# Kernel optimization log

Measured on AMD Instinct MI355X. Metric: run time of the kernel, lower is better.

Reference implementation:

```python
import jax, jax.numpy as jnp
import numpy as np

N, D = 8192, 4096
DIM_K = 4096

def setup_inputs() -> dict:
    key0 = jax.random.key(0)
    k1, k2, k3 = jax.random.split(key0, 3)
    return {
        "query": jax.random.normal(k1, (N, D), dtype=jnp.float32),
        "key": jax.random.normal(k2, (D, N), dtype=jnp.float32),
        "value": jax.random.normal(k3, (N, D), dtype=jnp.float32),
    }

def reference(query, key, value):
    # Faithful to the (buggy) torch module: ELEMENTWISE query * key.T,
    # scale by sqrt(dim_k), elementwise * value, softmax over dim=1
    # (F.softmax's implicit dim for a 2D tensor). The mask branch in the
    # original (`if x:`) cannot execute for multi-element tensors, so it
    # is omitted (mask=None path).
    scale = jnp.sqrt(jnp.float32(DIM_K))
    x = (query * key.T) / scale  # [N, D]
    x = x * value                # [N, D]
    return jax.nn.softmax(x, axis=1)
```

## Files before the change

### kernel.cpp

```cpp
#include <hip/hip_runtime.h>
#include <math.h>


static constexpr int NROW = 8192;
static constexpr int D    = 4096;
static constexpr int RPB  = 16;
static constexpr int TJ   = 256;
static constexpr int NT   = D / TJ;
static constexpr int LSTR = TJ + 4;

__global__ __launch_bounds__(1024, 2)
void sdp_softmax_kernel(const float* __restrict__ Q,
                        const float* __restrict__ K,
                        const float* __restrict__ V,
                        float* __restrict__ O)
{
    __shared__ float ldsK[2][RPB * LSTR];

    const int tid  = threadIdx.x;
    const int wv   = tid >> 6;
    const int lane = tid & 63;

    const int row0 = blockIdx.x * RPB;
    const int r    = row0 + wv;

    const float* qrow = Q + (size_t)r * D;
    const float* vrow = V + (size_t)r * D;
    float*       orow = O + (size_t)r * D;

    const int il = tid & 15;
    const int jg = tid >> 4;
    const float* kbase = K + (size_t)(4 * jg) * NROW + (size_t)row0 + il;

    float ka = kbase[0];
    float kb = kbase[NROW];
    float kc = kbase[2 * (size_t)NROW];
    float kd = kbase[3 * (size_t)NROW];
    *(float4*)&ldsK[0][il * LSTR + 4 * jg] = make_float4(ka, kb, kc, kd);
    {
        const float* p = kbase + (size_t)TJ * NROW;
        ka = p[0]; kb = p[NROW]; kc = p[2 * (size_t)NROW]; kd = p[3 * (size_t)NROW];
    }
    float4 qv = *(const float4*)(qrow + 4 * lane);
    float4 vv = *(const float4*)(vrow + 4 * lane);
    __syncthreads();

    float4 e0, e1, e2, e3, e4, e5, e6, e7,
           e8, e9, e10, e11, e12, e13, e14, e15;
    float s = 0.0f;

#define TILE_ITER(n, EV)                                                      \
    {                                                                         \
        const float4 kf = *(const float4*)&ldsK[(n) & 1][wv * LSTR + 4*lane]; \
        const float4 qc = qv, vc = vv;                                        \
        if ((n) + 1 < NT) {                                                   \
            *(float4*)&ldsK[((n) + 1) & 1][il * LSTR + 4 * jg] =              \
                make_float4(ka, kb, kc, kd);                                  \
            qv = *(const float4*)(qrow + ((n) + 1) * TJ + 4 * lane);          \
            vv = *(const float4*)(vrow + ((n) + 1) * TJ + 4 * lane);          \
        }                                                                     \
        if ((n) + 2 < NT) {                                                   \
            const float* p = kbase + (size_t)((n) + 2) * TJ * NROW;           \
            ka = p[0]; kb = p[NROW];                                          \
            kc = p[2 * (size_t)NROW]; kd = p[3 * (size_t)NROW];               \
        }                                                                     \
        EV.x = __expf(((qc.x * kf.x) * 0.015625f) * vc.x);                    \
        EV.y = __expf(((qc.y * kf.y) * 0.015625f) * vc.y);                    \
        EV.z = __expf(((qc.z * kf.z) * 0.015625f) * vc.z);                    \
        EV.w = __expf(((qc.w * kf.w) * 0.015625f) * vc.w);                    \
        s += (EV.x + EV.y) + (EV.z + EV.w);                                   \
        if ((n) + 1 < NT) __syncthreads();                                    \
        __builtin_amdgcn_sched_barrier(0);                                    \
    }

    TILE_ITER(0,  e0)  TILE_ITER(1,  e1)  TILE_ITER(2,  e2)  TILE_ITER(3,  e3)
    TILE_ITER(4,  e4)  TILE_ITER(5,  e5)  TILE_ITER(6,  e6)  TILE_ITER(7,  e7)
    TILE_ITER(8,  e8)  TILE_ITER(9,  e9)  TILE_ITER(10, e10) TILE_ITER(11, e11)
    TILE_ITER(12, e12) TILE_ITER(13, e13) TILE_ITER(14, e14) TILE_ITER(15, e15)
#undef TILE_ITER

    #pragma unroll
    for (int i = 1; i < 64; i <<= 1)
        s += __shfl_xor(s, i, 64);
    const float inv = 1.0f / s;

#define WRITE_TILE(n, EV)                                                     \
    {                                                                         \
        float4 xx = EV;                                                       \
        xx.x *= inv; xx.y *= inv; xx.z *= inv; xx.w *= inv;                   \
        *(float4*)(orow + (size_t)(n) * TJ + 4 * lane) = xx;                  \
    }

    WRITE_TILE(0,  e0)  WRITE_TILE(1,  e1)  WRITE_TILE(2,  e2)  WRITE_TILE(3,  e3)
    WRITE_TILE(4,  e4)  WRITE_TILE(5,  e5)  WRITE_TILE(6,  e6)  WRITE_TILE(7,  e7)
    WRITE_TILE(8,  e8)  WRITE_TILE(9,  e9)  WRITE_TILE(10, e10) WRITE_TILE(11, e11)
    WRITE_TILE(12, e12) WRITE_TILE(13, e13) WRITE_TILE(14, e14) WRITE_TILE(15, e15)
#undef WRITE_TILE
}

extern "C" void kernel_launch(void* const* d_in, const int* in_sizes, int n_in,
                              void* d_out, int out_size, void* d_ws, size_t ws_size,
                              hipStream_t stream) {
    const float* Q = (const float*)d_in[0];
    const float* K = (const float*)d_in[1];
    const float* V = (const float*)d_in[2];
    float* O = (float*)d_out;

    dim3 grid(NROW / RPB);
    dim3 block(1024);
    sdp_softmax_kernel<<<grid, block, 0, stream>>>(Q, K, V, O);
}
```

Before: 124.3 us.

## Pre-transpose K to bf16 workspace and stream rows with 4-deep prefetch

Adds a separate kernel that transposes K through LDS and stores it as bf16 in the workspace, so the main kernel can read K rows contiguously instead of doing a strided in-block transpose. The main kernel drops LDS and block-wide syncs, uses 256-thread blocks with a 4-tile register prefetch ring, and keeps the exponentials in bf16 registers to reduce register pressure. This adds an extra launch and a write-then-read of a 64MB intermediate. Rounding K and the stored exponentials to bf16 also lowers output precision.

```diff
diff --git a/kernel.cpp b/kernel.cpp
--- a/kernel.cpp
+++ b/kernel.cpp
@@ -4,91 +4,135 @@
 
 static constexpr int NROW = 8192;
 static constexpr int D    = 4096;
-static constexpr int RPB  = 16;
-static constexpr int TJ   = 256;
-static constexpr int NT   = D / TJ;
-static constexpr int LSTR = TJ + 4;
+static constexpr float SCL = 0.015625f;
 
-__global__ __launch_bounds__(1024, 2)
-void sdp_softmax_kernel(const float* __restrict__ Q,
-                        const float* __restrict__ K,
-                        const float* __restrict__ V,
-                        float* __restrict__ O)
+__device__ __forceinline__ unsigned short f2bf(float f) {
+    unsigned int b = __float_as_uint(f);
+    b = (b + 0x7FFFu + ((b >> 16) & 1u)) >> 16;
+    return (unsigned short)b;
+}
+__device__ __forceinline__ float bf2f(unsigned short u) {
+    return __uint_as_float(((unsigned int)u) << 16);
+}
+
+__global__ __launch_bounds__(256, 2)
+void kt_transpose_kernel(const float* __restrict__ K,
+                         unsigned short* __restrict__ KT)
 {
-    __shared__ float ldsK[2][RPB * LSTR];
+    __shared__ float lds[64][257];
+    const int t  = threadIdx.x;
+    const int jt = blockIdx.x & 63;
+    const int it = blockIdx.x >> 6;
+    const int j0 = jt * 64;
+    const int i0 = it * 256;
 
+    const int rr = t >> 6;
+    const int i4 = t & 63;
+    #pragma unroll
+    for (int s = 0; s < 16; ++s) {
+        const int jr = s * 4 + rr;
+        const float4 v =
+            *(const float4*)(K + (size_t)(j0 + jr) * NROW + i0 + 4 * i4);
+        *(float4*)&lds[jr][4 * i4] = v;
+    }
+    __syncthreads();
+
+    const int j4 = t & 15;
+    const int ir = t >> 4;
+    #pragma unroll
+    for (int sw = 0; sw < 16; ++sw) {
+        const int il = sw * 16 + ir;
+        ushort4 w;
+        w.x = f2bf(lds[4 * j4 + 0][il]);
+        w.y = f2bf(lds[4 * j4 + 1][il]);
+        w.z = f2bf(lds[4 * j4 + 2][il]);
+        w.w = f2bf(lds[4 * j4 + 3][il]);
+        *(ushort4*)(KT + (size_t)(i0 + il) * D + j0 + 4 * j4) = w;
+    }
+}
+
+__global__ __launch_bounds__(256, 4)
+void sdp_stream_kernel(const float* __restrict__ Q,
+                       const unsigned short* __restrict__ KT,
+                       const float* __restrict__ V,
+                       float* __restrict__ O)
+{
     const int tid  = threadIdx.x;
     const int wv   = tid >> 6;
     const int lane = tid & 63;
+    const int r    = blockIdx.x * 4 + wv;
 
-    const int row0 = blockIdx.x * RPB;
-    const int r    = row0 + wv;
+    const float*          qrow = Q  + (size_t)r * D;
+    const unsigned short* krow = KT + (size_t)r * D;
+    const float*          vrow = V  + (size_t)r * D;
+    float*                orow = O  + (size_t)r * D;
+    const int c0 = 4 * lane;
 
-    const float* qrow = Q + (size_t)r * D;
-    const float* vrow = V + (size_t)r * D;
-    float*       orow = O + (size_t)r * D;
+    float4  qA = *(const float4*)(qrow + 0 * 256 + c0);
+    ushort4 kA = *(const ushort4*)(krow + 0 * 256 + c0);
+    float4  vA = *(const float4*)(vrow + 0 * 256 + c0);
+    float4  qB = *(const float4*)(qrow + 1 * 256 + c0);
+    ushort4 kB = *(const ushort4*)(krow + 1 * 256 + c0);
+    float4  vB = *(const float4*)(vrow + 1 * 256 + c0);
+    float4  qC = *(const float4*)(qrow + 2 * 256 + c0);
+    ushort4 kC = *(const ushort4*)(krow + 2 * 256 + c0);
+    float4  vC = *(const float4*)(vrow + 2 * 256 + c0);
+    float4  qD = *(const float4*)(qrow + 3 * 256 + c0);
+    ushort4 kD = *(const ushort4*)(krow + 3 * 256 + c0);
+    float4  vD = *(const float4*)(vrow + 3 * 256 + c0);
 
-    const int il = tid & 15;
-    const int jg = tid >> 4;
-    const float* kbase = K + (size_t)(4 * jg) * NROW + (size_t)row0 + il;
-
-    float ka = kbase[0];
-    float kb = kbase[NROW];
-    float kc = kbase[2 * (size_t)NROW];
-    float kd = kbase[3 * (size_t)NROW];
-    *(float4*)&ldsK[0][il * LSTR + 4 * jg] = make_float4(ka, kb, kc, kd);
-    {
-        const float* p = kbase + (size_t)TJ * NROW;
-        ka = p[0]; kb = p[NROW]; kc = p[2 * (size_t)NROW]; kd = p[3 * (size_t)NROW];
-    }
-    float4 qv = *(const float4*)(qrow + 4 * lane);
-    float4 vv = *(const float4*)(vrow + 4 * lane);
-    __syncthreads();
-
-    float4 e0, e1, e2, e3, e4, e5, e6, e7,
-           e8, e9, e10, e11, e12, e13, e14, e15;
+    ushort4 e0, e1, e2, e3, e4, e5, e6, e7,
+            e8, e9, e10, e11, e12, e13, e14, e15;
     float s = 0.0f;
 
-#define TILE_ITER(n, EV)                                                      \
+#define BODY(t, ET, QS, KS, VS)                                               \
     {                                                                         \
-        const float4 kf = *(const float4*)&ldsK[(n) & 1][wv * LSTR + 4*lane]; \
-        const float4 qc = qv, vc = vv;                                        \
-        if ((n) + 1 < NT) {                                                   \
-            *(float4*)&ldsK[((n) + 1) & 1][il * LSTR + 4 * jg] =              \
-                make_float4(ka, kb, kc, kd);                                  \
-            qv = *(const float4*)(qrow + ((n) + 1) * TJ + 4 * lane);          \
-            vv = *(const float4*)(vrow + ((n) + 1) * TJ + 4 * lane);          \
+        const float4 qc = QS; const ushort4 kc = KS; const float4 vc = VS;    \
+        if ((t) + 4 < 16) {                                                   \
+            QS = *(const float4*)(qrow + ((t) + 4) * 256 + c0);               \
+            KS = *(const ushort4*)(krow + ((t) + 4) * 256 + c0);              \
+            VS = *(const float4*)(vrow + ((t) + 4) * 256 + c0);               \
         }                                                                     \
-        if ((n) + 2 < NT) {                                                   \
-            const float* p = kbase + (size_t)((n) + 2) * TJ * NROW;           \
-            ka = p[0]; kb = p[NROW];                                          \
-            kc = p[2 * (size_t)NROW]; kd = p[3 * (size_t)NROW];               \
-        }                                                                     \
-        EV.x = __expf(((qc.x * kf.x) * 0.015625f) * vc.x);                    \
-        EV.y = __expf(((qc.y * kf.y) * 0.015625f) * vc.y);                    \
-        EV.z = __expf(((qc.z * kf.z) * 0.015625f) * vc.z);                    \
-        EV.w = __expf(((qc.w * kf.w) * 0.015625f) * vc.w);                    \
-        s += (EV.x + EV.y) + (EV.z + EV.w);                                   \
-        if ((n) + 1 < NT) __syncthreads();                                    \
+        const float ex = __expf(((qc.x * bf2f(kc.x)) * SCL) * vc.x);          \
+        const float ey = __expf(((qc.y * bf2f(kc.y)) * SCL) * vc.y);          \
+        const float ez = __expf(((qc.z * bf2f(kc.z)) * SCL) * vc.z);          \
+        const float ew = __expf(((qc.w * bf2f(kc.w)) * SCL) * vc.w);          \
+        s += ((ex + ey) + (ez + ew));                                         \
+        ET.x = f2bf(ex); ET.y = f2bf(ey); ET.z = f2bf(ez); ET.w = f2bf(ew);   \
         __builtin_amdgcn_sched_barrier(0);                                    \
     }
 
-    TILE_ITER(0,  e0)  TILE_ITER(1,  e1)  TILE_ITER(2,  e2)  TILE_ITER(3,  e3)
-    TILE_ITER(4,  e4)  TILE_ITER(5,  e5)  TILE_ITER(6,  e6)  TILE_ITER(7,  e7)
-    TILE_ITER(8,  e8)  TILE_ITER(9,  e9)  TILE_ITER(10, e10) TILE_ITER(11, e11)
-    TILE_ITER(12, e12) TILE_ITER(13, e13) TILE_ITER(14, e14) TILE_ITER(15, e15)
-#undef TILE_ITER
+    BODY(0,  e0,  qA, kA, vA)
+    BODY(1,  e1,  qB, kB, vB)
+    BODY(2,  e2,  qC, kC, vC)
+    BODY(3,  e3,  qD, kD, vD)
+    BODY(4,  e4,  qA, kA, vA)
+    BODY(5,  e5,  qB, kB, vB)
+    BODY(6,  e6,  qC, kC, vC)
+    BODY(7,  e7,  qD, kD, vD)
+    BODY(8,  e8,  qA, kA, vA)
+    BODY(9,  e9,  qB, kB, vB)
+    BODY(10, e10, qC, kC, vC)
+    BODY(11, e11, qD, kD, vD)
+    BODY(12, e12, qA, kA, vA)
+    BODY(13, e13, qB, kB, vB)
+    BODY(14, e14, qC, kC, vC)
+    BODY(15, e15, qD, kD, vD)
+#undef BODY
 
     #pragma unroll
     for (int i = 1; i < 64; i <<= 1)
         s += __shfl_xor(s, i, 64);
     const float inv = 1.0f / s;
 
-#define WRITE_TILE(n, EV)                                                     \
+#define WRITE_TILE(t, ET)                                                     \
     {                                                                         \
-        float4 xx = EV;                                                       \
-        xx.x *= inv; xx.y *= inv; xx.z *= inv; xx.w *= inv;                   \
-        *(float4*)(orow + (size_t)(n) * TJ + 4 * lane) = xx;                  \
+        float4 xx;                                                            \
+        xx.x = bf2f(ET.x) * inv;                                              \
+        xx.y = bf2f(ET.y) * inv;                                              \
+        xx.z = bf2f(ET.z) * inv;                                              \
+        xx.w = bf2f(ET.w) * inv;                                              \
+        *(float4*)(orow + (size_t)(t) * 256 + c0) = xx;                       \
     }
 
     WRITE_TILE(0,  e0)  WRITE_TILE(1,  e1)  WRITE_TILE(2,  e2)  WRITE_TILE(3,  e3)
@@ -106,7 +150,7 @@
     const float* V = (const float*)d_in[2];
     float* O = (float*)d_out;
 
-    dim3 grid(NROW / RPB);
-    dim3 block(1024);
-    sdp_softmax_kernel<<<grid, block, 0, stream>>>(Q, K, V, O);
+    unsigned short* KT = (unsigned short*)d_ws;
+    kt_transpose_kernel<<<dim3(64 * 32), dim3(256), 0, stream>>>(K, KT);
+    sdp_stream_kernel<<<dim3(NROW / 4), dim3(256), 0, stream>>>(Q, KT, V, O);
 }
```

After: 140.3 us. +12.9%, slower.
